# Kernel tuning notes

Hardware: AMD Instinct MI355X
Metric: run time of the kernel (lower is better)

The kernel has to match this reference:

```python
import jax, jax.numpy as jnp
import numpy as np

DIM = 1024
NUM_HEADS = 16
DIM_PROJ = int(2 / 3 * 4 * DIM // 8 * 8)  # 2728, per source
EPS = 1e-5


def rms_norm(x, g):
    # NOTE: source computes sqrt(mean(x^2)) then divides by (rms + eps)
    rms = jnp.sqrt(jnp.mean(x * x, axis=-1, keepdims=True))
    return x / (rms + EPS) * g


def alibi_slopes(num_heads):
    base = (2.0 ** 8) ** (1.0 / num_heads)
    return jnp.asarray([1.0 / base ** (i + 1) for i in range(num_heads)], dtype=jnp.float32)


def setup_inputs() -> dict:
    key = jax.random.key(0)
    ks = jax.random.split(key, 7)
    B, T, C, P = 2, 2048, DIM, DIM_PROJ
    s = 0.02
    return {
        "x": jax.random.normal(ks[0], (B, T, C), dtype=jnp.float32),
        "g1": jnp.ones((C,), dtype=jnp.float32),
        "w_qkv": jax.random.normal(ks[1], (C, 3 * C), dtype=jnp.float32) * s,
        "w_o": jax.random.normal(ks[2], (C, C), dtype=jnp.float32) * s,
        "g2": jnp.ones((C,), dtype=jnp.float32),
        "W": jax.random.normal(ks[3], (C, P), dtype=jnp.float32) * s,
        "V": jax.random.normal(ks[4], (C, P), dtype=jnp.float32) * s,
        "W2": jax.random.normal(ks[5], (P, C), dtype=jnp.float32) * s,
    }


def reference(x, g1, w_qkv, w_o, g2, W, V, W2):
    B, T, C = x.shape
    H = NUM_HEADS
    Dh = C // H

    # --- attention sublayer ---
    h = rms_norm(x, g1)
    qkv = h @ w_qkv                              # [B,T,3C]
    q, k, v = jnp.split(qkv, 3, axis=-1)
    q = q.reshape(B, T, H, Dh).transpose(0, 2, 1, 3)  # [B,H,T,Dh]
    k = k.reshape(B, T, H, Dh).transpose(0, 2, 1, 3)
    v = v.reshape(B, T, H, Dh).transpose(0, 2, 1, 3)

    wei = jnp.einsum('bhqd,bhkd->bhqk', q, k)
    pos = jnp.arange(T)
    rel = (pos[None, :] - pos[:, None]).astype(jnp.float32)  # [T,T]
    m = alibi_slopes(H)[:, None, None]                        # [H,1,1]
    scale = C ** 0.5                                          # sqrt(dim), per source
    scores = wei / scale + m * rel
    causal = pos[None, :] <= pos[:, None]                     # [T,T]
    scores = jnp.where(causal[None, None], scores, -jnp.inf)
    attn = jax.nn.softmax(scores, axis=-1)

    out = jnp.einsum('bhqk,bhkd->bhqd', attn, v)
    concat = out.transpose(0, 2, 1, 3).reshape(B, T, C)
    x = concat @ w_o + x

    # --- SwiGLU sublayer ---
    h = rms_norm(x, g2)
    gated = jax.nn.silu(h @ W) * (h @ V)
    return gated @ W2 + x
```

## Files before the change

### kernel.cpp

```cpp
#include <hip/hip_runtime.h>
#include <math.h>

typedef __attribute__((ext_vector_type(8))) short bf16x8;
typedef __attribute__((ext_vector_type(4))) float f32x4;
typedef __attribute__((ext_vector_type(16))) float f32x16;

static __device__ __forceinline__ short f2bf(float x){
  union { float f; unsigned u; } a; a.f = x;
  unsigned r = a.u + 0x7fffu + ((a.u >> 16) & 1u);
  return (short)(r >> 16);
}

static __device__ __forceinline__ unsigned cvtpk(float lo, float hi){
  unsigned r; asm("v_cvt_pk_bf16_f32 %0, %1, %2" : "=v"(r) : "v"(lo), "v"(hi)); return r;
}

__global__ __launch_bounds__(256) void transpose_bf16_kernel(
    const float* __restrict__ in, short* __restrict__ out,
    int IR, int IC, int OR, int OC)
{
  __shared__ float tile[32][33];
  int i0 = blockIdx.x * 32;
  int j0 = blockIdx.y * 32;
  int tx = threadIdx.x, ty = threadIdx.y;
  #pragma unroll
  for (int r = 0; r < 32; r += 8){
    int j = j0 + ty + r, i = i0 + tx;
    tile[ty + r][tx] = (j < IR && i < IC) ? in[(size_t)j * IC + i] : 0.f;
  }
  __syncthreads();
  #pragma unroll
  for (int r = 0; r < 32; r += 8){
    int oi = i0 + ty + r, oj = j0 + tx;
    if (oi < OR && oj < OC) out[(size_t)oi * OC + oj] = f2bf(tile[tx][ty + r]);
  }
}

__global__ __launch_bounds__(256) void transpose_bb_kernel(
    const short* __restrict__ in, short* __restrict__ out)
{
  __shared__ short tile[32][33];
  int bh = blockIdx.z;
  int t0 = blockIdx.x * 32;
  int d0 = blockIdx.y * 32;
  int tx = threadIdx.x, ty = threadIdx.y;
  const short* src = in + ((size_t)bh * 2048 + t0) * 64 + d0;
  #pragma unroll
  for (int r = 0; r < 32; r += 8)
    tile[ty + r][tx] = src[(size_t)(ty + r) * 64 + tx];
  __syncthreads();
  short* dst = out + ((size_t)bh * 64 + d0) * 2048 + t0;
  #pragma unroll
  for (int r = 0; r < 32; r += 8)
    dst[(size_t)(ty + r) * 2048 + tx] = tile[tx][ty + r];
}

__global__ __launch_bounds__(256) void rmsnorm_kernel(
    const float* __restrict__ x, const float* __restrict__ g, short* __restrict__ out)
{
  int row = blockIdx.x, tid = threadIdx.x;
  const float4* xr = (const float4*)(x + (size_t)row * 1024);
  float4 v = xr[tid];
  float ss = v.x*v.x + v.y*v.y + v.z*v.z + v.w*v.w;
  #pragma unroll
  for (int m = 1; m < 64; m <<= 1) ss += __shfl_xor(ss, m, 64);
  __shared__ float sm[4];
  if ((tid & 63) == 0) sm[tid >> 6] = ss;
  __syncthreads();
  float tot = sm[0] + sm[1] + sm[2] + sm[3];
  float inv = 1.f / (sqrtf(tot * (1.f/1024.f)) + 1e-5f);
  float4 gv = ((const float4*)g)[tid];
  short4 o;
  o.x = f2bf(v.x * inv * gv.x);
  o.y = f2bf(v.y * inv * gv.y);
  o.z = f2bf(v.z * inv * gv.z);
  o.w = f2bf(v.w * inv * gv.w);
  *(short4*)(out + (size_t)row * 1024 + tid * 4) = o;
}

enum { EPI_F32 = 0, EPI_RESID = 1, EPI_QKV = 2, EPI_GATED = 3 };

template<int BM, int BN>
static __device__ __forceinline__ void dp_issue(
    const short* __restrict__ A, const short* __restrict__ Bt,
    short* __restrict__ lbuf, int K, int m0, int n0, int k0,
    int wave, int lane, int l)
{
  int g = (l * 8 + wave) * 64 + lane;
  const short* src;
  if (g < BM * 8){
    int row = g >> 3, cc = g & 7;
    src = A + (size_t)(m0 + row) * K + k0 + ((cc ^ (row & 7)) << 3);
  } else {
    int gb = g - BM * 8;
    int row = gb >> 3, cc = gb & 7;
    src = Bt + (size_t)(n0 + row) * K + k0 + ((cc ^ (row & 7)) << 3);
  }
  __builtin_amdgcn_global_load_lds((const __attribute__((address_space(1))) void*)src,
                                   (__attribute__((address_space(3))) void*)(lbuf + (size_t)g * 8),
                                   16, 0, 0);
}

template<int BM, int BN, int EPI>
__global__ __launch_bounds__(512, 2) void gemm_dp_kernel(
    const short* __restrict__ A, const short* __restrict__ Bt,
    int M, int N, int K,
    float* __restrict__ outF, short* __restrict__ outB,
    const float* __restrict__ resid, const float* __restrict__ Gprev,
    short* __restrict__ qb, short* __restrict__ kb, short* __restrict__ vb)
{
  constexpr int L  = (BM + BN) / 64;
  constexpr int WM = BM / 2, WN = BN / 4;
  constexpr int FR = WM / 16, FC = WN / 16;
  __shared__ short lds[2][(BM + BN) * 64];
  const int tid = threadIdx.x, lane = tid & 63, wave = tid >> 6;
  const int wr = wave >> 2, wc = wave & 3;
  const int la = lane & 15, lg = lane >> 4;

  int nbn = N / BN;
  int nwg = (M / BM) * nbn;
  int bid = blockIdx.x;
  int wg = ((nwg & 7) == 0) ? ((bid & 7) * (nwg >> 3) + (bid >> 3)) : bid;
  int m0 = (wg / nbn) * BM, n0 = (wg % nbn) * BN;

  f32x4 acc[FR][FC];
  #pragma unroll
  for (int i = 0; i < FR; ++i)
    #pragma unroll
    for (int j = 0; j < FC; ++j) acc[i][j] = f32x4{0.f, 0.f, 0.f, 0.f};

  const int NT = K >> 6;

  #pragma unroll
  for (int l = 0; l < L; ++l) dp_issue<BM, BN>(A, Bt, lds[0], K, m0, n0, 0,  wave, lane, l);
  #pragma unroll
  for (int l = 0; l < L; ++l) dp_issue<BM, BN>(A, Bt, lds[1], K, m0, n0, 64, wave, lane, l);

  for (int t = 0; t < NT; ++t){
    short* curb = lds[t & 1];
    if (t + 1 < NT){
      if constexpr (L == 8) asm volatile("s_waitcnt vmcnt(8)" ::: "memory");
      else                  asm volatile("s_waitcnt vmcnt(4)" ::: "memory");
    } else {
      asm volatile("s_waitcnt vmcnt(0)" ::: "memory");
    }
    __builtin_amdgcn_s_barrier();
    __builtin_amdgcn_sched_barrier(0);

    #pragma unroll
    for (int qr = 0; qr < FR / 4; ++qr){
      #pragma unroll
      for (int qc = 0; qc < FC / 2; ++qc){
        bf16x8 af[4][2], bfv[2][2];
        #pragma unroll
        for (int ii = 0; ii < 4; ++ii){
          int r = wr * WM + (qr * 4 + ii) * 16 + la;
          #pragma unroll
          for (int ks = 0; ks < 2; ++ks)
            af[ii][ks] = *(const bf16x8*)(curb + r * 64 + (((ks * 4 + lg) ^ (r & 7)) << 3));
        }
        #pragma unroll
        for (int jc = 0; jc < 2; ++jc){
          int rb = wc * WN + (qc * 2 + jc) * 16 + la;
          #pragma unroll
          for (int ks = 0; ks < 2; ++ks)
            bfv[jc][ks] = *(const bf16x8*)(curb + BM * 64 + rb * 64 + (((ks * 4 + lg) ^ (rb & 7)) << 3));
        }
        __builtin_amdgcn_s_setprio(1);
        #pragma unroll
        for (int ii = 0; ii < 4; ++ii)
          #pragma unroll
          for (int jc = 0; jc < 2; ++jc){
            acc[qr*4+ii][qc*2+jc] = __builtin_amdgcn_mfma_f32_16x16x32_bf16(
                af[ii][0], bfv[jc][0], acc[qr*4+ii][qc*2+jc], 0, 0, 0);
            acc[qr*4+ii][qc*2+jc] = __builtin_amdgcn_mfma_f32_16x16x32_bf16(
                af[ii][1], bfv[jc][1], acc[qr*4+ii][qc*2+jc], 0, 0, 0);
          }
        __builtin_amdgcn_s_setprio(0);
      }
    }
    __builtin_amdgcn_sched_barrier(0);
    __builtin_amdgcn_s_barrier();
    __builtin_amdgcn_sched_barrier(0);
    if (t + 2 < NT){
      #pragma unroll
      for (int l = 0; l < L; ++l)
        dp_issue<BM, BN>(A, Bt, curb, K, m0, n0, (t + 2) << 6, wave, lane, l);
    }
  }

  #pragma unroll
  for (int i = 0; i < FR; ++i){
    #pragma unroll
    for (int j = 0; j < FC; ++j){
      #pragma unroll
      for (int rr = 0; rr < 4; ++rr){
        int row = m0 + wr * WM + i * 16 + lg * 4 + rr;
        int col = n0 + wc * WN + j * 16 + la;
        float v = acc[i][j][rr];
        size_t idx = (size_t)row * N + col;
        if (EPI == EPI_F32){
          outF[idx] = v;
        } else if (EPI == EPI_RESID){
          outF[idx] = v + resid[idx];
        } else if (EPI == EPI_GATED){
          float gg = Gprev[idx];
          float s = gg / (1.f + __expf(-gg));
          outB[idx] = f2bf(s * v);
        } else {
          int which = col >> 10;
          int hh = (col & 1023) >> 6;
          int d = col & 63;
          int bb = row >> 11, tt = row & 2047;
          size_t o = (((size_t)(bb * 16 + hh) * 2048) + tt) * 64 + d;
          if (which == 0)      qb[o] = f2bf(v * 0.045084220f);
          else if (which == 1) kb[o] = f2bf(v);
          else                 vb[o] = f2bf(v);
        }
      }
    }
  }
}


#define KVLOAD(KF, VF, T_)                                                      \
  do {                                                                          \
    _Pragma("unroll")                                                           \
    for (int ks = 0; ks < 4; ++ks)                                              \
      KF[ks] = *(const bf16x8*)(Kg + ((size_t)((T_) * 32 + q32)) * 64 + ks * 16 + hi * 8); \
    _Pragma("unroll")                                                           \
    for (int dk = 0; dk < 4; ++dk)                                              \
      VF[dk] = *(const bf16x8*)(Vt + ((size_t)((dk >> 1) * 32 + q32)) * 2048 + (T_) * 32 + (dk & 1) * 16 + hi * 8); \
  } while (0)

#define PROC(CK, CV, T_, DOPF, NK, NV)                                          \
  do {                                                                          \
    f32x16 s;                                                                   \
    _Pragma("unroll") for (int i = 0; i < 16; ++i) s[i] = 0.f;                  \
    s = __builtin_amdgcn_mfma_f32_32x32x16_bf16(CK[0], qf[0], s, 0, 0, 0);      \
    s = __builtin_amdgcn_mfma_f32_32x32x16_bf16(CK[1], qf[1], s, 0, 0, 0);      \
    s = __builtin_amdgcn_mfma_f32_32x32x16_bf16(CK[2], qf[2], s, 0, 0, 0);      \
    s = __builtin_amdgcn_mfma_f32_32x32x16_bf16(CK[3], qf[3], s, 0, 0, 0);      \
    if (DOPF) KVLOAD(NK, NV, (T_) + 1);                                         \
    float sc[16];                                                               \
    _Pragma("unroll")                                                           \
    for (int r = 0; r < 16; ++r){                                               \
      int kvp = (T_) * 32 + (r & 3) + 8 * (r >> 2) + 4 * hi;                    \
      float vv = s[r] + slope2 * (float)(kvp - qpos);                           \
      sc[r] = (kvp <= qpos) ? vv : -1e30f;                                      \
    }                                                                           \
    float t8[8], t4[4];                                                         \
    _Pragma("unroll") for (int i = 0; i < 8; ++i) t8[i] = fmaxf(sc[i], sc[i + 8]); \
    _Pragma("unroll") for (int i = 0; i < 4; ++i) t4[i] = fmaxf(t8[i], t8[i + 4]); \
    float mx = fmaxf(fmaxf(t4[0], t4[1]), fmaxf(t4[2], t4[3]));                 \
    mx = fmaxf(mx, __shfl_xor(mx, 32, 64));                                     \
    if (!__all(mx <= m_run + 8.f)){                                             \
      float mnew = fmaxf(m_run, mx);                                            \
      float aL = exp2f(m_run - mnew);                                           \
      l_run *= aL;                                                              \
      m_run = mnew;                                                             \
      _Pragma("unroll")                                                         \
      for (int r = 0; r < 16; ++r){                                             \
        float aq = __shfl(aL, (r & 3) + 8 * (r >> 2) + 4 * hi, 64);             \
        o0[r] *= aq; o1[r] *= aq;                                               \
      }                                                                         \
    }                                                                           \
    float pr[16];                                                               \
    _Pragma("unroll")                                                           \
    for (int r = 0; r < 16; ++r) pr[r] = exp2f(sc[r] - m_run);                  \
    _Pragma("unroll") for (int i = 0; i < 8; ++i) t8[i] = pr[i] + pr[i + 8];    \
    _Pragma("unroll") for (int i = 0; i < 4; ++i) t4[i] = t8[i] + t8[i + 4];    \
    float ps = (t4[0] + t4[1]) + (t4[2] + t4[3]);                               \
    ps += __shfl_xor(ps, 32, 64);                                               \
    l_run += ps;                                                                \
    unsigned c0 = cvtpk(pr[0], pr[1]),   c1 = cvtpk(pr[2], pr[3]);              \
    unsigned c2 = cvtpk(pr[4], pr[5]),   c3 = cvtpk(pr[6], pr[7]);              \
    unsigned c4 = cvtpk(pr[8], pr[9]),   c5 = cvtpk(pr[10], pr[11]);            \
    unsigned c6 = cvtpk(pr[12], pr[13]), c7 = cvtpk(pr[14], pr[15]);            \
    unsigned x0 = (unsigned)__shfl_xor((int)c0, 32, 64), x1 = (unsigned)__shfl_xor((int)c1, 32, 64); \
    unsigned x2 = (unsigned)__shfl_xor((int)c2, 32, 64), x3 = (unsigned)__shfl_xor((int)c3, 32, 64); \
    unsigned x4 = (unsigned)__shfl_xor((int)c4, 32, 64), x5 = (unsigned)__shfl_xor((int)c5, 32, 64); \
    unsigned x6 = (unsigned)__shfl_xor((int)c6, 32, 64), x7 = (unsigned)__shfl_xor((int)c7, 32, 64); \
    union { unsigned u[4]; bf16x8 v; } pa0u, pa1u;                              \
    pa0u.u[0] = hi ? x2 : c0;  pa0u.u[1] = hi ? x3 : c1;                        \
    pa0u.u[2] = hi ? c2 : x0;  pa0u.u[3] = hi ? c3 : x1;                        \
    pa1u.u[0] = hi ? x6 : c4;  pa1u.u[1] = hi ? x7 : c5;                        \
    pa1u.u[2] = hi ? c6 : x4;  pa1u.u[3] = hi ? c7 : x5;                        \
    o0 = __builtin_amdgcn_mfma_f32_32x32x16_bf16(pa0u.v, CV[0], o0, 0, 0, 0);   \
    o0 = __builtin_amdgcn_mfma_f32_32x32x16_bf16(pa1u.v, CV[1], o0, 0, 0, 0);   \
    o1 = __builtin_amdgcn_mfma_f32_32x32x16_bf16(pa0u.v, CV[2], o1, 0, 0, 0);   \
    o1 = __builtin_amdgcn_mfma_f32_32x32x16_bf16(pa1u.v, CV[3], o1, 0, 0, 0);   \
  } while (0)

__global__ __launch_bounds__(256) void attn_kernel(
    const short* __restrict__ qb, const short* __restrict__ kb,
    const short* __restrict__ vtb, short* __restrict__ concat)
{
  const int T = 2048;
  int id = blockIdx.x;
  int bh = (id & 7) + 8 * ((id >> 3) & 3);
  int g  = id >> 5;
  int wave = threadIdx.x >> 6;
  int p = g * 4 + wave;
  int lane = threadIdx.x & 63;
  int q32 = lane & 31;
  int hi  = lane >> 5;
  int h = bh & 15, b = bh >> 4;

  const short* Q  = qb  + (size_t)bh * T * 64;
  const short* Kg = kb  + (size_t)bh * T * 64;
  const short* Vt = vtb + (size_t)bh * 64 * T;

  float slope2 = exp2f(-0.5f * (float)(h + 1)) * 1.44269504f;

  for (int hf = 0; hf < 2; ++hf){
    int j = hf ? (63 - p) : p;
    int q0 = j * 32;
    int qpos = q0 + q32;
    int nt = j + 1;

    bf16x8 qf[4];
    #pragma unroll
    for (int ks = 0; ks < 4; ++ks)
      qf[ks] = *(const bf16x8*)(Q + (size_t)qpos * 64 + ks * 16 + hi * 8);

    f32x16 o0, o1;
    #pragma unroll
    for (int i = 0; i < 16; ++i){ o0[i] = 0.f; o1[i] = 0.f; }
    float m_run = -1e30f, l_run = 0.f;

    bf16x8 kA[4], vA[4], kB[4], vB[4];
    KVLOAD(kA, vA, 0);

    int t = 0;
    while (1){
      PROC(kA, vA, t, (t + 1 < nt), kB, vB);
      ++t; if (t >= nt) break;
      PROC(kB, vB, t, (t + 1 < nt), kA, vA);
      ++t; if (t >= nt) break;
    }

    float linv = 1.f / l_run;
    #pragma unroll
    for (int r = 0; r < 16; ++r){
      int crow = (r & 3) + 8 * (r >> 2) + 4 * hi;
      float lq = __shfl(linv, crow, 64);
      size_t base = ((size_t)(b * 2048 + q0 + crow)) * 1024 + h * 64;
      concat[base + q32]      = f2bf(o0[r] * lq);
      concat[base + 32 + q32] = f2bf(o1[r] * lq);
    }
  }
}

extern "C" void kernel_launch(void* const* d_in, const int* in_sizes, int n_in,
                              void* d_out, int out_size, void* d_ws, size_t ws_size,
                              hipStream_t stream)
{
  (void)in_sizes; (void)n_in; (void)out_size; (void)ws_size;
  const float* x     = (const float*)d_in[0];
  const float* g1    = (const float*)d_in[1];
  const float* w_qkv = (const float*)d_in[2];
  const float* w_o   = (const float*)d_in[3];
  const float* g2    = (const float*)d_in[4];
  const float* W     = (const float*)d_in[5];
  const float* V     = (const float*)d_in[6];
  const float* W2    = (const float*)d_in[7];
  float* out = (float*)d_out;

  char* wsb = (char*)d_ws;
  size_t off = 0;
  auto alloc = [&](size_t bytes) -> void* {
    void* p = wsb + off;
    off += (bytes + 255) & ~(size_t)255;
    return p;
  };
  short* wqkvT = (short*)alloc((size_t)3072 * 1024 * 2);
  short* woT   = (short*)alloc((size_t)1024 * 1024 * 2);
  short* WT    = (short*)alloc((size_t)2816 * 1024 * 2);
  short* VT    = (short*)alloc((size_t)2816 * 1024 * 2);
  short* W2T   = (short*)alloc((size_t)1024 * 2816 * 2);
  short* h1    = (short*)alloc((size_t)4096 * 1024 * 2);
  short* qbuf  = (short*)alloc((size_t)4096 * 1024 * 2);
  short* kbuf  = (short*)alloc((size_t)4096 * 1024 * 2);
  short* vbuf  = (short*)alloc((size_t)4096 * 1024 * 2);
  short* vtbuf = (short*)alloc((size_t)4096 * 1024 * 2);
  short* conc  = (short*)alloc((size_t)4096 * 1024 * 2);
  float* x2    = (float*)alloc((size_t)4096 * 1024 * 4);
  short* h2    = (short*)alloc((size_t)4096 * 1024 * 2);
  float* G     = (float*)alloc((size_t)4096 * 2816 * 4);
  short* gated = (short*)alloc((size_t)4096 * 2816 * 2);

  dim3 tb(32, 8);
  hipLaunchKernelGGL(transpose_bf16_kernel, dim3(96, 32), tb, 0, stream, w_qkv, wqkvT, 1024, 3072, 3072, 1024);
  hipLaunchKernelGGL(transpose_bf16_kernel, dim3(32, 32), tb, 0, stream, w_o,   woT,   1024, 1024, 1024, 1024);
  hipLaunchKernelGGL(transpose_bf16_kernel, dim3(88, 32), tb, 0, stream, W,     WT,    1024, 2728, 2816, 1024);
  hipLaunchKernelGGL(transpose_bf16_kernel, dim3(88, 32), tb, 0, stream, V,     VT,    1024, 2728, 2816, 1024);
  hipLaunchKernelGGL(transpose_bf16_kernel, dim3(32, 88), tb, 0, stream, W2,    W2T,   2728, 1024, 1024, 2816);

  hipLaunchKernelGGL(rmsnorm_kernel, dim3(4096), dim3(256), 0, stream, x, g1, h1);

  hipLaunchKernelGGL((gemm_dp_kernel<256, 256, EPI_QKV>), dim3(192), dim3(512), 0, stream,
                     h1, wqkvT, 4096, 3072, 1024,
                     (float*)nullptr, (short*)nullptr, (const float*)nullptr, (const float*)nullptr,
                     qbuf, kbuf, vbuf);

  hipLaunchKernelGGL(transpose_bb_kernel, dim3(64, 2, 32), tb, 0, stream, vbuf, vtbuf);

  hipLaunchKernelGGL(attn_kernel, dim3(256), dim3(256), 0, stream, qbuf, kbuf, vtbuf, conc);

  hipLaunchKernelGGL((gemm_dp_kernel<128, 128, EPI_RESID>), dim3(256), dim3(512), 0, stream,
                     conc, woT, 4096, 1024, 1024,
                     x2, (short*)nullptr, x, (const float*)nullptr,
                     (short*)nullptr, (short*)nullptr, (short*)nullptr);

  hipLaunchKernelGGL(rmsnorm_kernel, dim3(4096), dim3(256), 0, stream, x2, g2, h2);

  hipLaunchKernelGGL((gemm_dp_kernel<256, 256, EPI_F32>), dim3(176), dim3(512), 0, stream,
                     h2, WT, 4096, 2816, 1024,
                     G, (short*)nullptr, (const float*)nullptr, (const float*)nullptr,
                     (short*)nullptr, (short*)nullptr, (short*)nullptr);

  hipLaunchKernelGGL((gemm_dp_kernel<256, 256, EPI_GATED>), dim3(176), dim3(512), 0, stream,
                     h2, VT, 4096, 2816, 1024,
                     (float*)nullptr, gated, (const float*)nullptr, G,
                     (short*)nullptr, (short*)nullptr, (short*)nullptr);

  hipLaunchKernelGGL((gemm_dp_kernel<128, 128, EPI_RESID>), dim3(256), dim3(512), 0, stream,
                     gated, W2T, 4096, 1024, 2816,
                     out, (short*)nullptr, x2, (const float*)nullptr,
                     (short*)nullptr, (short*)nullptr, (short*)nullptr);
}
```

Before: 295.4 us.

## Split attention KV range across waves with LDS merge of partial softmax

Result: slower. 315.3 us (+6.7%).

```diff
diff --git a/kernel.cpp b/kernel.cpp
--- a/kernel.cpp
+++ b/kernel.cpp
@@ -233,21 +233,26 @@
       VF[dk] = *(const bf16x8*)(Vt + ((size_t)((dk >> 1) * 32 + q32)) * 2048 + (T_) * 32 + (dk & 1) * 16 + hi * 8); \
   } while (0)
 
+#define CBASE(r) ((float)(((r) & 3) + 8 * ((r) >> 2)))
+#define CBI(r)   ((((r) & 3) + 8 * ((r) >> 2)))
+
 #define PROC(CK, CV, T_, DOPF, NK, NV)                                          \
   do {                                                                          \
-    f32x16 s;                                                                   \
-    _Pragma("unroll") for (int i = 0; i < 16; ++i) s[i] = 0.f;                  \
-    s = __builtin_amdgcn_mfma_f32_32x32x16_bf16(CK[0], qf[0], s, 0, 0, 0);      \
-    s = __builtin_amdgcn_mfma_f32_32x32x16_bf16(CK[1], qf[1], s, 0, 0, 0);      \
-    s = __builtin_amdgcn_mfma_f32_32x32x16_bf16(CK[2], qf[2], s, 0, 0, 0);      \
-    s = __builtin_amdgcn_mfma_f32_32x32x16_bf16(CK[3], qf[3], s, 0, 0, 0);      \
-    if (DOPF) KVLOAD(NK, NV, (T_) + 1);                                         \
+    f32x16 sS;                                                                  \
+    _Pragma("unroll") for (int i = 0; i < 16; ++i) sS[i] = 0.f;                 \
+    sS = __builtin_amdgcn_mfma_f32_32x32x16_bf16(CK[0], qf[0], sS, 0, 0, 0);    \
+    sS = __builtin_amdgcn_mfma_f32_32x32x16_bf16(CK[1], qf[1], sS, 0, 0, 0);    \
+    sS = __builtin_amdgcn_mfma_f32_32x32x16_bf16(CK[2], qf[2], sS, 0, 0, 0);    \
+    sS = __builtin_amdgcn_mfma_f32_32x32x16_bf16(CK[3], qf[3], sS, 0, 0, 0);    \
+    if (DOPF) KVLOAD(NK, NV, (T_) + 4);                                         \
+    float bb = slope2 * (float)((T_) * 32 + 4 * hi - qpos);                     \
     float sc[16];                                                               \
     _Pragma("unroll")                                                           \
-    for (int r = 0; r < 16; ++r){                                               \
-      int kvp = (T_) * 32 + (r & 3) + 8 * (r >> 2) + 4 * hi;                    \
-      float vv = s[r] + slope2 * (float)(kvp - qpos);                           \
-      sc[r] = (kvp <= qpos) ? vv : -1e30f;                                      \
+    for (int r = 0; r < 16; ++r) sc[r] = (sS[r] + bb) + slope2 * CBASE(r);      \
+    if ((T_) == j){                                                             \
+      _Pragma("unroll")                                                         \
+      for (int r = 0; r < 16; ++r)                                              \
+        sc[r] = (CBI(r) + 4 * hi <= q32) ? sc[r] : -1e30f;                      \
     }                                                                           \
     float t8[8], t4[4];                                                         \
     _Pragma("unroll") for (int i = 0; i < 8; ++i) t8[i] = fmaxf(sc[i], sc[i + 8]); \
@@ -261,7 +266,7 @@
       m_run = mnew;                                                             \
       _Pragma("unroll")                                                         \
       for (int r = 0; r < 16; ++r){                                             \
-        float aq = __shfl(aL, (r & 3) + 8 * (r >> 2) + 4 * hi, 64);             \
+        float aq = __shfl(aL, CBI(r) + 4 * hi, 64);                             \
         o0[r] *= aq; o1[r] *= aq;                                               \
       }                                                                         \
     }                                                                           \
@@ -299,56 +304,88 @@
   const int T = 2048;
   int id = blockIdx.x;
   int bh = (id & 7) + 8 * ((id >> 3) & 3);
-  int g  = id >> 5;
-  int wave = threadIdx.x >> 6;
-  int p = g * 4 + wave;
-  int lane = threadIdx.x & 63;
+  int j  = 63 - (id >> 5);
+  int tid = threadIdx.x;
+  int s = tid >> 6;
+  int lane = tid & 63;
   int q32 = lane & 31;
   int hi  = lane >> 5;
   int h = bh & 15, b = bh >> 4;
 
+  __shared__ float part[4][16][64][2];
+  __shared__ float mlbuf[4][64][2];
+
   const short* Q  = qb  + (size_t)bh * T * 64;
   const short* Kg = kb  + (size_t)bh * T * 64;
   const short* Vt = vtb + (size_t)bh * 64 * T;
 
   float slope2 = exp2f(-0.5f * (float)(h + 1)) * 1.44269504f;
 
-  for (int hf = 0; hf < 2; ++hf){
-    int j = hf ? (63 - p) : p;
-    int q0 = j * 32;
-    int qpos = q0 + q32;
-    int nt = j + 1;
-
-    bf16x8 qf[4];
+  int q0 = j * 32;
+  int qpos = q0 + q32;
+
+  bf16x8 qf[4];
+  #pragma unroll
+  for (int ks = 0; ks < 4; ++ks)
+    qf[ks] = *(const bf16x8*)(Q + (size_t)qpos * 64 + ks * 16 + hi * 8);
+
+  f32x16 o0, o1;
+  #pragma unroll
+  for (int i = 0; i < 16; ++i){ o0[i] = 0.f; o1[i] = 0.f; }
+  float m_run = -1e30f, l_run = 0.f;
+
+  if (s <= j){
+    bf16x8 kA[4], vA[4], kB[4], vB[4];
+    KVLOAD(kA, vA, s);
+    int t = s;
+    while (true){
+      PROC(kA, vA, t, (t + 4 <= j), kB, vB);
+      t += 4; if (t > j) break;
+      PROC(kB, vB, t, (t + 4 <= j), kA, vA);
+      t += 4; if (t > j) break;
+    }
+  }
+
+  #pragma unroll
+  for (int r2 = 0; r2 < 8; ++r2){
+    part[s][r2][lane][0]     = o0[2 * r2];
+    part[s][r2][lane][1]     = o0[2 * r2 + 1];
+    part[s][r2 + 8][lane][0] = o1[2 * r2];
+    part[s][r2 + 8][lane][1] = o1[2 * r2 + 1];
+  }
+  mlbuf[s][lane][0] = m_run;
+  mlbuf[s][lane][1] = l_run;
+  __syncthreads();
+
+  #pragma unroll
+  for (int k = 0; k < 4; ++k){
+    int r2 = s * 4 + k;
+    int ri = r2 * 2;
+    int rb = ri & 15;
+    int colb = (ri < 16) ? 0 : 32;
+    int crow0 = CBI(rb) + 4 * hi;
+    int crow1 = crow0 + 1;
+
+    float m0v = -1e30f, m1v = -1e30f;
     #pragma unroll
-    for (int ks = 0; ks < 4; ++ks)
-      qf[ks] = *(const bf16x8*)(Q + (size_t)qpos * 64 + ks * 16 + hi * 8);
-
-    f32x16 o0, o1;
+    for (int w = 0; w < 4; ++w){
+      m0v = fmaxf(m0v, mlbuf[w][crow0][0]);
+      m1v = fmaxf(m1v, mlbuf[w][crow1][0]);
+    }
+    float l0v = 0.f, l1v = 0.f, vx = 0.f, vy = 0.f;
     #pragma unroll
-    for (int i = 0; i < 16; ++i){ o0[i] = 0.f; o1[i] = 0.f; }
-    float m_run = -1e30f, l_run = 0.f;
-
-    bf16x8 kA[4], vA[4], kB[4], vB[4];
-    KVLOAD(kA, vA, 0);
-
-    int t = 0;
-    while (1){
-      PROC(kA, vA, t, (t + 1 < nt), kB, vB);
-      ++t; if (t >= nt) break;
-      PROC(kB, vB, t, (t + 1 < nt), kA, vA);
-      ++t; if (t >= nt) break;
-    }
-
-    float linv = 1.f / l_run;
-    #pragma unroll
-    for (int r = 0; r < 16; ++r){
-      int crow = (r & 3) + 8 * (r >> 2) + 4 * hi;
-      float lq = __shfl(linv, crow, 64);
-      size_t base = ((size_t)(b * 2048 + q0 + crow)) * 1024 + h * 64;
-      concat[base + q32]      = f2bf(o0[r] * lq);
-      concat[base + 32 + q32] = f2bf(o1[r] * lq);
-    }
+    for (int w = 0; w < 4; ++w){
+      float a0 = exp2f(mlbuf[w][crow0][0] - m0v);
+      float a1 = exp2f(mlbuf[w][crow1][0] - m1v);
+      l0v += a0 * mlbuf[w][crow0][1];
+      l1v += a1 * mlbuf[w][crow1][1];
+      vx  += a0 * part[w][r2][lane][0];
+      vy  += a1 * part[w][r2][lane][1];
+    }
+    size_t base0 = ((size_t)(b * 2048 + q0 + crow0)) * 1024 + h * 64 + colb + q32;
+    size_t base1 = ((size_t)(b * 2048 + q0 + crow1)) * 1024 + h * 64 + colb + q32;
+    concat[base0] = f2bf(vx / l0v);
+    concat[base1] = f2bf(vy / l1v);
   }
 }
 
@@ -406,7 +443,7 @@
 
   hipLaunchKernelGGL(transpose_bb_kernel, dim3(64, 2, 32), tb, 0, stream, vbuf, vtbuf);
 
-  hipLaunchKernelGGL(attn_kernel, dim3(256), dim3(256), 0, stream, qbuf, kbuf, vtbuf, conc);
+  hipLaunchKernelGGL(attn_kernel, dim3(2048), dim3(256), 0, stream, qbuf, kbuf, vtbuf, conc);
 
   hipLaunchKernelGGL((gemm_dp_kernel<128, 128, EPI_RESID>), dim3(256), dim3(512), 0, stream,
                      conc, woT, 4096, 1024, 1024,
```

## Split attention work per query block, mask only diagonal tile, shrink GEMM tiles

Applied to the files above, without the earlier changes.

Result: slower. 302.1 us (+2.3%).

```diff
diff --git a/kernel.cpp b/kernel.cpp
--- a/kernel.cpp
+++ b/kernel.cpp
@@ -139,8 +139,9 @@
   for (int t = 0; t < NT; ++t){
     short* curb = lds[t & 1];
     if (t + 1 < NT){
-      if constexpr (L == 8) asm volatile("s_waitcnt vmcnt(8)" ::: "memory");
-      else                  asm volatile("s_waitcnt vmcnt(4)" ::: "memory");
+      if constexpr (L == 8)      asm volatile("s_waitcnt vmcnt(8)" ::: "memory");
+      else if constexpr (L == 6) asm volatile("s_waitcnt vmcnt(6)" ::: "memory");
+      else                       asm volatile("s_waitcnt vmcnt(4)" ::: "memory");
     } else {
       asm volatile("s_waitcnt vmcnt(0)" ::: "memory");
     }
@@ -233,21 +234,26 @@
       VF[dk] = *(const bf16x8*)(Vt + ((size_t)((dk >> 1) * 32 + q32)) * 2048 + (T_) * 32 + (dk & 1) * 16 + hi * 8); \
   } while (0)
 
+#define CBASE(r) ((float)(((r) & 3) + 8 * ((r) >> 2)))
+#define CBI(r)   ((((r) & 3) + 8 * ((r) >> 2)))
+
 #define PROC(CK, CV, T_, DOPF, NK, NV)                                          \
   do {                                                                          \
-    f32x16 s;                                                                   \
-    _Pragma("unroll") for (int i = 0; i < 16; ++i) s[i] = 0.f;                  \
-    s = __builtin_amdgcn_mfma_f32_32x32x16_bf16(CK[0], qf[0], s, 0, 0, 0);      \
-    s = __builtin_amdgcn_mfma_f32_32x32x16_bf16(CK[1], qf[1], s, 0, 0, 0);      \
-    s = __builtin_amdgcn_mfma_f32_32x32x16_bf16(CK[2], qf[2], s, 0, 0, 0);      \
-    s = __builtin_amdgcn_mfma_f32_32x32x16_bf16(CK[3], qf[3], s, 0, 0, 0);      \
+    f32x16 sS;                                                                  \
+    _Pragma("unroll") for (int i = 0; i < 16; ++i) sS[i] = 0.f;                 \
+    sS = __builtin_amdgcn_mfma_f32_32x32x16_bf16(CK[0], qf[0], sS, 0, 0, 0);    \
+    sS = __builtin_amdgcn_mfma_f32_32x32x16_bf16(CK[1], qf[1], sS, 0, 0, 0);    \
+    sS = __builtin_amdgcn_mfma_f32_32x32x16_bf16(CK[2], qf[2], sS, 0, 0, 0);    \
+    sS = __builtin_amdgcn_mfma_f32_32x32x16_bf16(CK[3], qf[3], sS, 0, 0, 0);    \
     if (DOPF) KVLOAD(NK, NV, (T_) + 1);                                         \
+    float bb = slope2 * (float)((T_) * 32 + 4 * hi - qpos);                     \
     float sc[16];                                                               \
     _Pragma("unroll")                                                           \
-    for (int r = 0; r < 16; ++r){                                               \
-      int kvp = (T_) * 32 + (r & 3) + 8 * (r >> 2) + 4 * hi;                    \
-      float vv = s[r] + slope2 * (float)(kvp - qpos);                           \
-      sc[r] = (kvp <= qpos) ? vv : -1e30f;                                      \
+    for (int r = 0; r < 16; ++r) sc[r] = (sS[r] + bb) + slope2 * CBASE(r);      \
+    if ((T_) == j){                                                             \
+      _Pragma("unroll")                                                         \
+      for (int r = 0; r < 16; ++r)                                              \
+        sc[r] = (CBI(r) + 4 * hi <= q32) ? sc[r] : -1e30f;                      \
     }                                                                           \
     float t8[8], t4[4];                                                         \
     _Pragma("unroll") for (int i = 0; i < 8; ++i) t8[i] = fmaxf(sc[i], sc[i + 8]); \
@@ -261,7 +267,7 @@
       m_run = mnew;                                                             \
       _Pragma("unroll")                                                         \
       for (int r = 0; r < 16; ++r){                                             \
-        float aq = __shfl(aL, (r & 3) + 8 * (r >> 2) + 4 * hi, 64);             \
+        float aq = __shfl(aL, CBI(r) + 4 * hi, 64);                             \
         o0[r] *= aq; o1[r] *= aq;                                               \
       }                                                                         \
     }                                                                           \
@@ -298,10 +304,10 @@
 {
   const int T = 2048;
   int id = blockIdx.x;
-  int bh = (id & 7) + 8 * ((id >> 3) & 3);
-  int g  = id >> 5;
+  int grp = id & 7;
+  int j   = 63 - (id >> 3);
   int wave = threadIdx.x >> 6;
-  int p = g * 4 + wave;
+  int bh = grp * 4 + wave;
   int lane = threadIdx.x & 63;
   int q32 = lane & 31;
   int hi  = lane >> 5;
@@ -313,42 +319,39 @@
 
   float slope2 = exp2f(-0.5f * (float)(h + 1)) * 1.44269504f;
 
-  for (int hf = 0; hf < 2; ++hf){
-    int j = hf ? (63 - p) : p;
-    int q0 = j * 32;
-    int qpos = q0 + q32;
-    int nt = j + 1;
-
-    bf16x8 qf[4];
-    #pragma unroll
-    for (int ks = 0; ks < 4; ++ks)
-      qf[ks] = *(const bf16x8*)(Q + (size_t)qpos * 64 + ks * 16 + hi * 8);
-
-    f32x16 o0, o1;
-    #pragma unroll
-    for (int i = 0; i < 16; ++i){ o0[i] = 0.f; o1[i] = 0.f; }
-    float m_run = -1e30f, l_run = 0.f;
-
-    bf16x8 kA[4], vA[4], kB[4], vB[4];
-    KVLOAD(kA, vA, 0);
-
-    int t = 0;
-    while (1){
-      PROC(kA, vA, t, (t + 1 < nt), kB, vB);
-      ++t; if (t >= nt) break;
-      PROC(kB, vB, t, (t + 1 < nt), kA, vA);
-      ++t; if (t >= nt) break;
-    }
-
-    float linv = 1.f / l_run;
-    #pragma unroll
-    for (int r = 0; r < 16; ++r){
-      int crow = (r & 3) + 8 * (r >> 2) + 4 * hi;
-      float lq = __shfl(linv, crow, 64);
-      size_t base = ((size_t)(b * 2048 + q0 + crow)) * 1024 + h * 64;
-      concat[base + q32]      = f2bf(o0[r] * lq);
-      concat[base + 32 + q32] = f2bf(o1[r] * lq);
-    }
+  int q0 = j * 32;
+  int qpos = q0 + q32;
+  int nt = j + 1;
+
+  bf16x8 qf[4];
+  #pragma unroll
+  for (int ks = 0; ks < 4; ++ks)
+    qf[ks] = *(const bf16x8*)(Q + (size_t)qpos * 64 + ks * 16 + hi * 8);
+
+  f32x16 o0, o1;
+  #pragma unroll
+  for (int i = 0; i < 16; ++i){ o0[i] = 0.f; o1[i] = 0.f; }
+  float m_run = -1e30f, l_run = 0.f;
+
+  bf16x8 kA[4], vA[4], kB[4], vB[4];
+  KVLOAD(kA, vA, 0);
+
+  int t = 0;
+  while (1){
+    PROC(kA, vA, t, (t + 1 < nt), kB, vB);
+    ++t; if (t >= nt) break;
+    PROC(kB, vB, t, (t + 1 < nt), kA, vA);
+    ++t; if (t >= nt) break;
+  }
+
+  float linv = 1.f / l_run;
+  #pragma unroll
+  for (int r = 0; r < 16; ++r){
+    int crow = CBI(r) + 4 * hi;
+    float lq = __shfl(linv, crow, 64);
+    size_t base = ((size_t)(b * 2048 + q0 + crow)) * 1024 + h * 64;
+    concat[base + q32]      = f2bf(o0[r] * lq);
+    concat[base + 32 + q32] = f2bf(o1[r] * lq);
   }
 }
 
@@ -399,14 +402,14 @@
 
   hipLaunchKernelGGL(rmsnorm_kernel, dim3(4096), dim3(256), 0, stream, x, g1, h1);
 
-  hipLaunchKernelGGL((gemm_dp_kernel<256, 256, EPI_QKV>), dim3(192), dim3(512), 0, stream,
+  hipLaunchKernelGGL((gemm_dp_kernel<256, 128, EPI_QKV>), dim3(384), dim3(512), 0, stream,
                      h1, wqkvT, 4096, 3072, 1024,
                      (float*)nullptr, (short*)nullptr, (const float*)nullptr, (const float*)nullptr,
                      qbuf, kbuf, vbuf);
 
   hipLaunchKernelGGL(transpose_bb_kernel, dim3(64, 2, 32), tb, 0, stream, vbuf, vtbuf);
 
-  hipLaunchKernelGGL(attn_kernel, dim3(256), dim3(256), 0, stream, qbuf, kbuf, vtbuf, conc);
+  hipLaunchKernelGGL(attn_kernel, dim3(512), dim3(256), 0, stream, qbuf, kbuf, vtbuf, conc);
 
   hipLaunchKernelGGL((gemm_dp_kernel<128, 128, EPI_RESID>), dim3(256), dim3(512), 0, stream,
                      conc, woT, 4096, 1024, 1024,
@@ -415,12 +418,12 @@
 
   hipLaunchKernelGGL(rmsnorm_kernel, dim3(4096), dim3(256), 0, stream, x2, g2, h2);
 
-  hipLaunchKernelGGL((gemm_dp_kernel<256, 256, EPI_F32>), dim3(176), dim3(512), 0, stream,
+  hipLaunchKernelGGL((gemm_dp_kernel<256, 128, EPI_F32>), dim3(352), dim3(512), 0, stream,
                      h2, WT, 4096, 2816, 1024,
                      G, (short*)nullptr, (const float*)nullptr, (const float*)nullptr,
                      (short*)nullptr, (short*)nullptr, (short*)nullptr);
 
-  hipLaunchKernelGGL((gemm_dp_kernel<256, 256, EPI_GATED>), dim3(176), dim3(512), 0, stream,
+  hipLaunchKernelGGL((gemm_dp_kernel<256, 128, EPI_GATED>), dim3(352), dim3(512), 0, stream,
                      h2, VT, 4096, 2816, 1024,
                      (float*)nullptr, gated, (const float*)nullptr, G,
                      (short*)nullptr, (short*)nullptr, (short*)nullptr);
```
